# Kernel tuning notes

Measured on AMD Instinct MI355X. Metric: run time of the kernel, lower is better.

Reference implementation:

```python
import jax, jax.numpy as jnp
import numpy as np

B, N, C_IN = 8, 2048, 3
D = 64            # graph-conv feature dim
SPARSE_K = 8      # k_neighbors(16) * sparse_ratio(0.5)
LEVELS = 3        # wavelet_levels
H1, H2 = 256, 128 # fusion hidden dims

def _lin(key, fan_in, fan_out):
    k1, k2 = jax.random.split(key)
    s = 1.0 / np.sqrt(fan_in)
    W = jax.random.uniform(k1, (fan_in, fan_out), minval=-s, maxval=s, dtype=jnp.float32)
    b = jax.random.uniform(k2, (fan_out,), minval=-s, maxval=s, dtype=jnp.float32)
    return W, b

def setup_inputs() -> dict:
    key = jax.random.key(0)
    ks = jax.random.split(key, 12)
    x = jax.random.normal(ks[0], (B, N, C_IN), dtype=jnp.float32)
    W1, b1 = _lin(ks[1], C_IN, D)          # feature_transform
    W2, b2 = _lin(ks[2], 2 * D, D)         # edge_conv
    Ws1, bs1 = _lin(ks[3], C_IN, 64)       # suppressor layer 1
    Ws2, bs2 = _lin(ks[4], 64, LEVELS)     # suppressor layer 2
    Wf1, bf1 = _lin(ks[5], D * LEVELS, H1) # fusion
    Wf2, bf2 = _lin(ks[6], H1, H2)
    Wf3, bf3 = _lin(ks[7], H2, C_IN)
    ones = jnp.ones; zeros = jnp.zeros
    return {
        'x': x,
        'W1': W1, 'b1': b1, 'g1': ones((D,), jnp.float32), 'be1': zeros((D,), jnp.float32),
        'W2': W2, 'b2': b2, 'g2': ones((D,), jnp.float32), 'be2': zeros((D,), jnp.float32),
        'Ws1': Ws1, 'bs1': bs1, 'Ws2': Ws2, 'bs2': bs2,
        'Wf1': Wf1, 'bf1': bf1, 'gf1': ones((H1,), jnp.float32), 'bef1': zeros((H1,), jnp.float32),
        'Wf2': Wf2, 'bf2': bf2, 'gf2': ones((H2,), jnp.float32), 'bef2': zeros((H2,), jnp.float32),
        'Wf3': Wf3, 'bf3': bf3,
    }

def _leaky(v):
    return jnp.where(v > 0, v, 0.2 * v)

def reference(x, W1, b1, g1, be1, W2, b2, g2, be2, Ws1, bs1, Ws2, bs2,
              Wf1, bf1, gf1, bef1, Wf2, bf2, gf2, bef2, Wf3, bf3):
    # ---- AdaptiveSparseGraphConv ----
    # feature transform + eval-mode BN (running mean 0 / var 1 -> affine)
    feat = _leaky((x @ W1 + b1) * g1 + be1)                     # [B,N,D]
    # KNN via squared distances (monotonic in true cdist)
    x2 = jnp.sum(x * x, axis=-1)                                # [B,N]
    d2 = x2[:, :, None] + x2[:, None, :] - 2.0 * jnp.einsum('bnc,bmc->bnm', x, x)
    _, idx = jax.lax.top_k(-d2, SPARSE_K)                       # [B,N,k] nearest
    neighbor = jax.vmap(lambda f, i: f[i])(feat, idx)           # [B,N,k,D]
    edge = jnp.concatenate(
        [jnp.broadcast_to(feat[:, :, None, :], neighbor.shape), neighbor], axis=-1)  # [B,N,k,2D]
    conv = _leaky((edge @ W2 + b2) * g2 + be2)                  # [B,N,k,D]
    agg = jnp.max(conv, axis=2)                                 # [B,N,D]
    # ---- AdaptiveFrequencySupressor (per-point wavelet-level weights) ----
    fw = jax.nn.sigmoid(jax.nn.relu(x @ Ws1 + bs1) @ Ws2 + bs2) # [B,N,LEVELS]
    # frequency-adaptive multi-level weighting, concat across levels
    multi = (agg[:, :, None, :] * fw[:, :, :, None]).reshape(B, N, LEVELS * D)  # [B,N,LEVELS*D]
    # ---- EnhancedMultiScaleFusion (eval: dropout off, BN affine) ----
    h = _leaky((multi @ Wf1 + bf1) * gf1 + bef1)
    h = _leaky((h @ Wf2 + bf2) * gf2 + bef2)
    delta = h @ Wf3 + bf3                                       # [B,N,3]
    # ---- residual regularized output ----
    return x + 0.1 * delta
```

## Files before the change

### kernel.cpp

```cpp
#include <hip/hip_runtime.h>
#include <hip/hip_bf16.h>
#include <math.h>

#define BB   8
#define NN   2048
#define BN   16384
#define KNB  8

__device__ __forceinline__ float leaky(float v){ return v > 0.f ? v : 0.2f*v; }

__device__ __forceinline__ ushort f2bf(float f){
    unsigned u = __float_as_uint(f);
    return (ushort)((u + 0x7FFFu + ((u >> 16) & 1u)) >> 16);
}
__device__ __forceinline__ float bf2f(ushort h){
    return __uint_as_float(((unsigned)h) << 16);
}

using bf16x8 = __attribute__((ext_vector_type(8))) short;
using f32x16 = __attribute__((ext_vector_type(16))) float;

__global__ __launch_bounds__(256) void k_pq(
    const float* __restrict__ x,
    const float* __restrict__ W1, const float* __restrict__ b1,
    const float* __restrict__ g1, const float* __restrict__ be1,
    const float* __restrict__ W2,
    const float* __restrict__ Wf1, const float* __restrict__ Wf2,
    float* __restrict__ P, ushort* __restrict__ Qb,
    ushort* __restrict__ Wf1T, ushort* __restrict__ Wf2T)
{
    int t = threadIdx.x;
    int bid = blockIdx.x;
    if (bid >= 256) {
        if (bid < 280) {
            int base = (bid - 256) * 2048 + t * 8;
            #pragma unroll
            for (int j = 0; j < 8; ++j) {
                int e = base + j;
                int n = e / 192, k = e % 192;
                Wf1T[e] = f2bf(Wf1[k*256 + n]);
            }
        } else {
            int base = (bid - 280) * 2048 + t * 8;
            #pragma unroll
            for (int j = 0; j < 8; ++j) {
                int e = base + j;
                int n = e / 256, k = e % 256;
                Wf2T[e] = f2bf(Wf2[k*128 + n]);
            }
        }
        return;
    }

    __shared__ float F_s[64*66];
    __shared__ float W_s[32*132];

    int rb = bid * 64;

    {
        int d = t & 63, g = t >> 6;
        float w0 = W1[d], w1 = W1[64+d], w2 = W1[128+d];
        float bb = b1[d], gg = g1[d], ee = be1[d];
        #pragma unroll 4
        for (int i = 0; i < 16; ++i) {
            int r = g*16 + i;
            const float* xp = &x[(rb + r)*3];
            float f = xp[0]*w0 + xp[1]*w1 + xp[2]*w2 + bb;
            f = leaky(f*gg + ee);
            F_s[r*66 + d] = f;
        }
    }

    int tx = t & 15, ty = t >> 4;
    float acc[4][8];
    #pragma unroll
    for (int i = 0; i < 4; ++i)
        #pragma unroll
        for (int j = 0; j < 8; ++j) acc[i][j] = 0.f;

    for (int k0 = 0; k0 < 64; k0 += 32) {
        __syncthreads();
        #pragma unroll
        for (int it = 0; it < 2; ++it) {
            int i2 = t + it*256;
            int k = i2 >> 4, c8 = (i2 & 15) * 8;
            const float* src = &W2[(k0 + k + (c8 >= 64 ? 64 : 0))*64 + (c8 & 63)];
            *(float4*)&W_s[k*132 + c8]     = *(const float4*)src;
            *(float4*)&W_s[k*132 + c8 + 4] = *(const float4*)(src + 4);
        }
        __syncthreads();
        #pragma unroll 4
        for (int kk = 0; kk < 32; ++kk) {
            float a[4];
            #pragma unroll
            for (int i = 0; i < 4; ++i) a[i] = F_s[(ty*4 + i)*66 + k0 + kk];
            float4 wA = *(const float4*)&W_s[kk*132 + tx*8];
            float4 wB = *(const float4*)&W_s[kk*132 + tx*8 + 4];
            #pragma unroll
            for (int i = 0; i < 4; ++i) {
                acc[i][0] = fmaf(a[i], wA.x, acc[i][0]);
                acc[i][1] = fmaf(a[i], wA.y, acc[i][1]);
                acc[i][2] = fmaf(a[i], wA.z, acc[i][2]);
                acc[i][3] = fmaf(a[i], wA.w, acc[i][3]);
                acc[i][4] = fmaf(a[i], wB.x, acc[i][4]);
                acc[i][5] = fmaf(a[i], wB.y, acc[i][5]);
                acc[i][6] = fmaf(a[i], wB.z, acc[i][6]);
                acc[i][7] = fmaf(a[i], wB.w, acc[i][7]);
            }
        }
    }

    #pragma unroll
    for (int i = 0; i < 4; ++i) {
        int r = rb + ty*4 + i;
        if (tx < 8) {
            *(float4*)&P[r*64 + tx*8]     = make_float4(acc[i][0], acc[i][1], acc[i][2], acc[i][3]);
            *(float4*)&P[r*64 + tx*8 + 4] = make_float4(acc[i][4], acc[i][5], acc[i][6], acc[i][7]);
        } else {
            union { ushort u[8]; uint4 v; } pk;
            #pragma unroll
            for (int j = 0; j < 8; ++j) pk.u[j] = f2bf(acc[i][j]);
            *(uint4*)&Qb[r*64 + (tx - 8)*8] = pk.v;
        }
    }
}

#define CE64(a, b) { bool c_ = (b) < (a); unsigned long long mn_ = c_ ? (b) : (a); \
                     unsigned long long mx_ = c_ ? (a) : (b); (a) = mn_; (b) = mx_; }

__global__ __launch_bounds__(1024, 8) void k_knn(const float* __restrict__ x, int* __restrict__ idxo)
{
    __shared__ __align__(16) char smem[65536];
    float4*   sp  = (float4*)smem;
    unsigned* khi = (unsigned*)smem;
    unsigned* klo = (unsigned*)(smem + 32768);

    int t = threadIdx.x;
    int b = blockIdx.x >> 6;
    int qbase = (blockIdx.x & 63) * 32;
    int q = t & 31, seg = t >> 5;

    for (int i = t; i < NN; i += 1024) {
        float a = x[(b*NN + i)*3 + 0];
        float c = x[(b*NN + i)*3 + 1];
        float e = x[(b*NN + i)*3 + 2];
        sp[i] = make_float4(a, c, e, a*a + c*c + e*e);
    }
    __syncthreads();

    float4 qv = sp[qbase + q];

    unsigned long long R[8];
    #pragma unroll
    for (int j = 0; j < 8; ++j) R[j] = 0xFFFFFFFFFFFFFFFFull;

    int m0 = seg * 64;
    #pragma unroll 2
    for (int g = 0; g < 8; ++g) {
        unsigned long long S[8];
        #pragma unroll
        for (int jj = 0; jj < 8; ++jj) {
            int m = m0 + g*8 + jj;
            float4 v = sp[m];
            float s = qv.x*v.x; s = fmaf(qv.y, v.y, s); s = fmaf(qv.z, v.z, s);
            float d2 = fmaf(-2.f, s, qv.w + v.w);
            unsigned u = __float_as_uint(fmaxf(d2, 0.f));
            S[jj] = ((unsigned long long)u << 32) | (unsigned)m;
        }
        CE64(S[0],S[1]); CE64(S[2],S[3]); CE64(S[4],S[5]); CE64(S[6],S[7]);
        CE64(S[0],S[2]); CE64(S[1],S[3]); CE64(S[4],S[6]); CE64(S[5],S[7]);
        CE64(S[1],S[2]); CE64(S[5],S[6]);
        CE64(S[0],S[4]); CE64(S[1],S[5]); CE64(S[2],S[6]); CE64(S[3],S[7]);
        CE64(S[2],S[4]); CE64(S[3],S[5]);
        CE64(S[1],S[2]); CE64(S[3],S[4]); CE64(S[5],S[6]);
        #pragma unroll
        for (int j = 0; j < 8; ++j) {
            unsigned long long bb = S[7-j];
            R[j] = R[j] < bb ? R[j] : bb;
        }
        CE64(R[0],R[4]); CE64(R[1],R[5]); CE64(R[2],R[6]); CE64(R[3],R[7]);
        CE64(R[0],R[2]); CE64(R[1],R[3]); CE64(R[4],R[6]); CE64(R[5],R[7]);
        CE64(R[0],R[1]); CE64(R[2],R[3]); CE64(R[4],R[5]); CE64(R[6],R[7]);
    }

    __syncthreads();
    #pragma unroll
    for (int j = 0; j < 8; ++j) {
        khi[j*1024 + t] = (unsigned)(R[j] >> 32);
        klo[j*1024 + t] = (unsigned)R[j];
    }

    for (int L = 32; L >= 2; L >>= 1) {
        __syncthreads();
        unsigned long long A[8], Bv[8];
        int p = t >> 5;
        bool active = (p < (L >> 1));
        if (active) {
            int rowA = (2*p)*32 + q, rowB = (2*p + 1)*32 + q;
            #pragma unroll
            for (int j = 0; j < 8; ++j) {
                A[j]  = ((unsigned long long)khi[j*1024 + rowA] << 32) | klo[j*1024 + rowA];
                Bv[j] = ((unsigned long long)khi[j*1024 + rowB] << 32) | klo[j*1024 + rowB];
            }
        }
        __syncthreads();
        if (active) {
            unsigned long long C[8];
            #pragma unroll
            for (int j = 0; j < 8; ++j) {
                unsigned long long bb = Bv[7-j];
                C[j] = A[j] < bb ? A[j] : bb;
            }
            CE64(C[0],C[4]); CE64(C[1],C[5]); CE64(C[2],C[6]); CE64(C[3],C[7]);
            CE64(C[0],C[2]); CE64(C[1],C[3]); CE64(C[4],C[6]); CE64(C[5],C[7]);
            CE64(C[0],C[1]); CE64(C[2],C[3]); CE64(C[4],C[5]); CE64(C[6],C[7]);
            if (L > 2) {
                int rowO = p*32 + q;
                #pragma unroll
                for (int j = 0; j < 8; ++j) {
                    khi[j*1024 + rowO] = (unsigned)(C[j] >> 32);
                    klo[j*1024 + rowO] = (unsigned)C[j];
                }
            } else {
                #pragma unroll
                for (int j = 0; j < 8; ++j)
                    idxo[(b*NN + qbase + q)*KNB + j] = b*NN + (int)(C[j] & 0xFFFFFFFFu);
            }
        }
    }
}

__global__ __launch_bounds__(256) void k_agg(
    const float* __restrict__ x,
    const float* __restrict__ P, const ushort* __restrict__ Qb,
    const int* __restrict__ idx,
    const float* __restrict__ Ws1, const float* __restrict__ bs1,
    const float* __restrict__ Ws2, const float* __restrict__ bs2,
    const float* __restrict__ b2, const float* __restrict__ g2,
    const float* __restrict__ be2,
    ushort* __restrict__ multi)
{
    int lane = threadIdx.x & 63;
    int p = blockIdx.x * 4 + (threadIdx.x >> 6);

    float x0 = x[p*3+0], x1 = x[p*3+1], x2 = x[p*3+2];
    float h = fmaxf(x0*Ws1[lane] + x1*Ws1[64+lane] + x2*Ws1[128+lane] + bs1[lane], 0.f);
    float s[3];
    #pragma unroll
    for (int l = 0; l < 3; ++l) {
        float v = h * Ws2[lane*3 + l];
        #pragma unroll
        for (int off = 32; off; off >>= 1) v += __shfl_xor(v, off, 64);
        s[l] = v + bs2[l];
    }
    float fw0 = 1.f/(1.f + expf(-s[0]));
    float fw1 = 1.f/(1.f + expf(-s[1]));
    float fw2 = 1.f/(1.f + expf(-s[2]));

    float Pv = P[p*64 + lane] + b2[lane];
    float g = g2[lane], be = be2[lane];
    float mx = -1e30f;
    #pragma unroll
    for (int j = 0; j < KNB; ++j) {
        int nb = idx[p*KNB + j];
        float qv = bf2f(Qb[nb*64 + lane]);
        float v = (Pv + qv) * g + be;
        mx = fmaxf(mx, leaky(v));
    }
    multi[p*192 + lane]       = f2bf(mx * fw0);
    multi[p*192 + 64  + lane] = f2bf(mx * fw1);
    multi[p*192 + 128 + lane] = f2bf(mx * fw2);
}

__global__ __launch_bounds__(256) void k_h1(
    const ushort* __restrict__ multi, const ushort* __restrict__ Wf1T,
    const float* __restrict__ bf1, const float* __restrict__ gf1,
    const float* __restrict__ bef1, ushort* __restrict__ h1)
{
    __shared__ ushort A_s[128*72];
    __shared__ ushort B_s[64*72];

    int t = threadIdx.x, w = t >> 6, lane = t & 63;
    int rb = blockIdx.x * 128, cb = blockIdx.y * 64;

    f32x16 acc[2];
    #pragma unroll
    for (int i = 0; i < 16; ++i) { acc[0][i] = 0.f; acc[1][i] = 0.f; }

    for (int k0 = 0; k0 < 192; k0 += 64) {
        #pragma unroll
        for (int it = 0; it < 4; ++it) {
            int i = t + it*256; int r = i >> 3, kq = (i & 7)*8;
            *(uint4*)&A_s[r*72 + kq] = *(const uint4*)&multi[(rb + r)*192 + k0 + kq];
        }
        #pragma unroll
        for (int it = 0; it < 2; ++it) {
            int i = t + it*256; int n = i >> 3, kq = (i & 7)*8;
            *(uint4*)&B_s[n*72 + kq] = *(const uint4*)&Wf1T[(cb + n)*192 + k0 + kq];
        }
        __syncthreads();
        int row = w*32 + (lane & 31);
        int kb = (lane >> 5)*8;
        #pragma unroll
        for (int s = 0; s < 4; ++s) {
            bf16x8 a  = *(const bf16x8*)&A_s[row*72 + s*16 + kb];
            bf16x8 b0 = *(const bf16x8*)&B_s[(lane & 31)*72 + s*16 + kb];
            bf16x8 b1 = *(const bf16x8*)&B_s[(32 + (lane & 31))*72 + s*16 + kb];
            acc[0] = __builtin_amdgcn_mfma_f32_32x32x16_bf16(a, b0, acc[0], 0, 0, 0);
            acc[1] = __builtin_amdgcn_mfma_f32_32x32x16_bf16(a, b1, acc[1], 0, 0, 0);
        }
        __syncthreads();
    }

    #pragma unroll
    for (int nb = 0; nb < 2; ++nb) {
        int c = cb + nb*32 + (lane & 31);
        float bv = bf1[c], gv = gf1[c], ev = bef1[c];
        #pragma unroll
        for (int r16 = 0; r16 < 16; ++r16) {
            int rr = (r16 & 3) + 8*(r16 >> 2) + 4*(lane >> 5);
            float v = leaky((acc[nb][r16] + bv)*gv + ev);
            h1[(rb + w*32 + rr)*256 + c] = f2bf(v);
        }
    }
}

__global__ __launch_bounds__(256) void k_h2out(
    const ushort* __restrict__ h1, const ushort* __restrict__ Wf2T,
    const float* __restrict__ bf2, const float* __restrict__ gf2,
    const float* __restrict__ bef2,
    const float* __restrict__ Wf3, const float* __restrict__ bf3,
    const float* __restrict__ x, float* __restrict__ out)
{
    __shared__ ushort A_s[128*72];
    __shared__ ushort B_s[128*72];

    int t = threadIdx.x, w = t >> 6, lane = t & 63;
    int rb = blockIdx.x * 128;

    f32x16 acc[4];
    #pragma unroll
    for (int nb = 0; nb < 4; ++nb)
        #pragma unroll
        for (int i = 0; i < 16; ++i) acc[nb][i] = 0.f;

    for (int k0 = 0; k0 < 256; k0 += 64) {
        #pragma unroll
        for (int it = 0; it < 4; ++it) {
            int i = t + it*256; int r = i >> 3, kq = (i & 7)*8;
            *(uint4*)&A_s[r*72 + kq] = *(const uint4*)&h1[(rb + r)*256 + k0 + kq];
        }
        #pragma unroll
        for (int it = 0; it < 4; ++it) {
            int i = t + it*256; int n = i >> 3, kq = (i & 7)*8;
            *(uint4*)&B_s[n*72 + kq] = *(const uint4*)&Wf2T[n*256 + k0 + kq];
        }
        __syncthreads();
        int row = w*32 + (lane & 31);
        int kb = (lane >> 5)*8;
        #pragma unroll
        for (int s = 0; s < 4; ++s) {
            bf16x8 a = *(const bf16x8*)&A_s[row*72 + s*16 + kb];
            #pragma unroll
            for (int nb = 0; nb < 4; ++nb) {
                bf16x8 b = *(const bf16x8*)&B_s[(nb*32 + (lane & 31))*72 + s*16 + kb];
                acc[nb] = __builtin_amdgcn_mfma_f32_32x32x16_bf16(a, b, acc[nb], 0, 0, 0);
            }
        }
        __syncthreads();
    }

    float bv[4], gv[4], ev[4], w3[4][3];
    #pragma unroll
    for (int nb = 0; nb < 4; ++nb) {
        int c = nb*32 + (lane & 31);
        bv[nb] = bf2[c]; gv[nb] = gf2[c]; ev[nb] = bef2[c];
        #pragma unroll
        for (int l = 0; l < 3; ++l) w3[nb][l] = Wf3[c*3 + l];
    }
    float b30 = bf3[0], b31 = bf3[1], b32 = bf3[2];

    #pragma unroll
    for (int r16 = 0; r16 < 16; ++r16) {
        float d0 = 0.f, d1 = 0.f, d2 = 0.f;
        #pragma unroll
        for (int nb = 0; nb < 4; ++nb) {
            float v = leaky((acc[nb][r16] + bv[nb])*gv[nb] + ev[nb]);
            d0 = fmaf(v, w3[nb][0], d0);
            d1 = fmaf(v, w3[nb][1], d1);
            d2 = fmaf(v, w3[nb][2], d2);
        }
        #pragma unroll
        for (int off = 16; off; off >>= 1) {
            d0 += __shfl_xor(d0, off, 64);
            d1 += __shfl_xor(d1, off, 64);
            d2 += __shfl_xor(d2, off, 64);
        }
        int row = rb + w*32 + (r16 & 3) + 8*(r16 >> 2) + 4*(lane >> 5);
        int l = lane & 31;
        if (l < 3) {
            float dl = (l == 0) ? d0 : (l == 1 ? d1 : d2);
            float bl = (l == 0) ? b30 : (l == 1 ? b31 : b32);
            out[row*3 + l] = x[row*3 + l] + 0.1f*(dl + bl);
        }
    }
}

extern "C" void kernel_launch(void* const* d_in, const int* in_sizes, int n_in,
                              void* d_out, int out_size, void* d_ws, size_t ws_size,
                              hipStream_t stream)
{
    const float* x    = (const float*)d_in[0];
    const float* W1   = (const float*)d_in[1];
    const float* b1   = (const float*)d_in[2];
    const float* g1   = (const float*)d_in[3];
    const float* be1  = (const float*)d_in[4];
    const float* W2   = (const float*)d_in[5];
    const float* b2   = (const float*)d_in[6];
    const float* g2   = (const float*)d_in[7];
    const float* be2  = (const float*)d_in[8];
    const float* Ws1  = (const float*)d_in[9];
    const float* bs1  = (const float*)d_in[10];
    const float* Ws2  = (const float*)d_in[11];
    const float* bs2  = (const float*)d_in[12];
    const float* Wf1  = (const float*)d_in[13];
    const float* bf1  = (const float*)d_in[14];
    const float* gf1  = (const float*)d_in[15];
    const float* bef1 = (const float*)d_in[16];
    const float* Wf2  = (const float*)d_in[17];
    const float* bf2  = (const float*)d_in[18];
    const float* gf2  = (const float*)d_in[19];
    const float* bef2 = (const float*)d_in[20];
    const float* Wf3  = (const float*)d_in[21];
    const float* bf3  = (const float*)d_in[22];
    float* out = (float*)d_out;

    char* ws = (char*)d_ws;
    int*    idx   = (int*)   (ws + 0);
    ushort* Wf1T  = (ushort*)(ws + (1u << 20));
    ushort* Wf2T  = (ushort*)(ws + (1u << 20) + (512u << 10));
    float*  P     = (float*) (ws + (2u  << 20));
    ushort* Qb    = (ushort*)(ws + (6u  << 20));
    ushort* multi = (ushort*)(ws + (8u  << 20));
    ushort* h1    = (ushort*)(ws + (14u << 20));

    k_pq<<<296, 256, 0, stream>>>(x, W1, b1, g1, be1, W2, Wf1, Wf2, P, Qb, Wf1T, Wf2T);
    k_knn<<<BB*64, 1024, 0, stream>>>(x, idx);
    k_agg<<<BN/4, 256, 0, stream>>>(x, P, Qb, idx, Ws1, bs1, Ws2, bs2, b2, g2, be2, multi);
    k_h1<<<dim3(BN/128, 4), 256, 0, stream>>>(multi, Wf1T, bf1, gf1, bef1, h1);
    k_h2out<<<dim3(BN/128, 1), 256, 0, stream>>>(h1, Wf2T, bf2, gf2, bef2, Wf3, bf3, x, out);
}
```

Before: 176.7 us.

## Fuse aggregation, fusion MLP layers and output into one kernel

Merges the neighbor-max aggregation, the first fusion GEMM, the second GEMM and the output projection into a single kernel that handles 64 rows per block and keeps the multi-level features and h1 in shared memory. This removes the global writes and reads of the intermediate multi and h1 tensors and two kernel launches. In exchange each block uses about 60KB of LDS, which limits occupancy. Every block also reloads the full Wf1T and Wf2T weights, and the aggregation phase now runs serially over 16 rows per wave.

New measurement: 172.1 us. 2.6% less time.

```diff
diff --git a/kernel.cpp b/kernel.cpp
--- a/kernel.cpp
+++ b/kernel.cpp
@@ -230,7 +230,7 @@
     }
 }
 
-__global__ __launch_bounds__(256) void k_agg(
+__global__ __launch_bounds__(256) void k_fuse(
     const float* __restrict__ x,
     const float* __restrict__ P, const ushort* __restrict__ Qb,
     const int* __restrict__ idx,
@@ -238,157 +238,146 @@
     const float* __restrict__ Ws2, const float* __restrict__ bs2,
     const float* __restrict__ b2, const float* __restrict__ g2,
     const float* __restrict__ be2,
-    ushort* __restrict__ multi)
+    const ushort* __restrict__ Wf1T, const float* __restrict__ bf1,
+    const float* __restrict__ gf1, const float* __restrict__ bef1,
+    const ushort* __restrict__ Wf2T, const float* __restrict__ bf2,
+    const float* __restrict__ gf2, const float* __restrict__ bef2,
+    const float* __restrict__ Wf3, const float* __restrict__ bf3,
+    float* __restrict__ out)
 {
-    int lane = threadIdx.x & 63;
-    int p = blockIdx.x * 4 + (threadIdx.x >> 6);
-
-    float x0 = x[p*3+0], x1 = x[p*3+1], x2 = x[p*3+2];
-    float h = fmaxf(x0*Ws1[lane] + x1*Ws1[64+lane] + x2*Ws1[128+lane] + bs1[lane], 0.f);
-    float s[3];
-    #pragma unroll
-    for (int l = 0; l < 3; ++l) {
-        float v = h * Ws2[lane*3 + l];
-        #pragma unroll
-        for (int off = 32; off; off >>= 1) v += __shfl_xor(v, off, 64);
-        s[l] = v + bs2[l];
-    }
-    float fw0 = 1.f/(1.f + expf(-s[0]));
-    float fw1 = 1.f/(1.f + expf(-s[1]));
-    float fw2 = 1.f/(1.f + expf(-s[2]));
-
-    float Pv = P[p*64 + lane] + b2[lane];
-    float g = g2[lane], be = be2[lane];
-    float mx = -1e30f;
-    #pragma unroll
-    for (int j = 0; j < KNB; ++j) {
-        int nb = idx[p*KNB + j];
-        float qv = bf2f(Qb[nb*64 + lane]);
-        float v = (Pv + qv) * g + be;
-        mx = fmaxf(mx, leaky(v));
-    }
-    multi[p*192 + lane]       = f2bf(mx * fw0);
-    multi[p*192 + 64  + lane] = f2bf(mx * fw1);
-    multi[p*192 + 128 + lane] = f2bf(mx * fw2);
-}
-
-__global__ __launch_bounds__(256) void k_h1(
-    const ushort* __restrict__ multi, const ushort* __restrict__ Wf1T,
-    const float* __restrict__ bf1, const float* __restrict__ gf1,
-    const float* __restrict__ bef1, ushort* __restrict__ h1)
-{
-    __shared__ ushort A_s[128*72];
-    __shared__ ushort B_s[64*72];
+    __shared__ __align__(16) char smem[60928];
+    ushort* A_s  = (ushort*)smem;
+    ushort* B_s  = (ushort*)(smem + 25600);
+    ushort* h1_s = (ushort*)smem;
+    ushort* B2_s = (ushort*)(smem + 40960);
+    float*  pd   = (float*) (smem + 59392);
 
     int t = threadIdx.x, w = t >> 6, lane = t & 63;
-    int rb = blockIdx.x * 128, cb = blockIdx.y * 64;
-
-    f32x16 acc[2];
-    #pragma unroll
-    for (int i = 0; i < 16; ++i) { acc[0][i] = 0.f; acc[1][i] = 0.f; }
+    int rb = blockIdx.x * 64;
+
+    {
+        float ws1a = Ws1[lane], ws1b = Ws1[64+lane], ws1c = Ws1[128+lane];
+        float bs1v = bs1[lane];
+        float ws2a = Ws2[lane*3+0], ws2b = Ws2[lane*3+1], ws2c = Ws2[lane*3+2];
+        float bs20 = bs2[0], bs21 = bs2[1], bs22 = bs2[2];
+        float g2v = g2[lane], be2v = be2[lane], b2v = b2[lane];
+        for (int i = 0; i < 16; ++i) {
+            int r = w*16 + i, p = rb + r;
+            float x0 = x[p*3+0], x1 = x[p*3+1], x2 = x[p*3+2];
+            float h = fmaxf(fmaf(x2, ws1c, fmaf(x1, ws1b, fmaf(x0, ws1a, bs1v))), 0.f);
+            float s0 = h*ws2a, s1 = h*ws2b, s2 = h*ws2c;
+            #pragma unroll
+            for (int off = 32; off; off >>= 1) {
+                s0 += __shfl_xor(s0, off, 64);
+                s1 += __shfl_xor(s1, off, 64);
+                s2 += __shfl_xor(s2, off, 64);
+            }
+            float fw0 = 1.f/(1.f + expf(-(s0 + bs20)));
+            float fw1 = 1.f/(1.f + expf(-(s1 + bs21)));
+            float fw2 = 1.f/(1.f + expf(-(s2 + bs22)));
+            float Pv = P[p*64 + lane] + b2v;
+            float mx = -1e30f;
+            #pragma unroll
+            for (int j = 0; j < KNB; ++j) {
+                int nb = idx[p*KNB + j];
+                float qv = bf2f(Qb[nb*64 + lane]);
+                mx = fmaxf(mx, leaky((Pv + qv)*g2v + be2v));
+            }
+            A_s[r*200 + lane]       = f2bf(mx * fw0);
+            A_s[r*200 + 64 + lane]  = f2bf(mx * fw1);
+            A_s[r*200 + 128 + lane] = f2bf(mx * fw2);
+        }
+    }
+
+    int rg = w >> 1;
+    int nh = (w & 1) * 128;
+    int l31 = lane & 31, kb = (lane >> 5) * 8;
+    int row = rg*32 + l31;
+
+    f32x16 acc[4];
+    #pragma unroll
+    for (int n2 = 0; n2 < 4; ++n2)
+        #pragma unroll
+        for (int i = 0; i < 16; ++i) acc[n2][i] = 0.f;
 
     for (int k0 = 0; k0 < 192; k0 += 64) {
-        #pragma unroll
-        for (int it = 0; it < 4; ++it) {
-            int i = t + it*256; int r = i >> 3, kq = (i & 7)*8;
-            *(uint4*)&A_s[r*72 + kq] = *(const uint4*)&multi[(rb + r)*192 + k0 + kq];
-        }
-        #pragma unroll
-        for (int it = 0; it < 2; ++it) {
-            int i = t + it*256; int n = i >> 3, kq = (i & 7)*8;
-            *(uint4*)&B_s[n*72 + kq] = *(const uint4*)&Wf1T[(cb + n)*192 + k0 + kq];
-        }
-        __syncthreads();
-        int row = w*32 + (lane & 31);
-        int kb = (lane >> 5)*8;
+        __syncthreads();
+        #pragma unroll
+        for (int it = 0; it < 8; ++it) {
+            int i = t + it*256;
+            int n = i >> 3, kq = (i & 7)*8;
+            *(uint4*)&B_s[n*72 + kq] = *(const uint4*)&Wf1T[n*192 + k0 + kq];
+        }
+        __syncthreads();
         #pragma unroll
         for (int s = 0; s < 4; ++s) {
-            bf16x8 a  = *(const bf16x8*)&A_s[row*72 + s*16 + kb];
-            bf16x8 b0 = *(const bf16x8*)&B_s[(lane & 31)*72 + s*16 + kb];
-            bf16x8 b1 = *(const bf16x8*)&B_s[(32 + (lane & 31))*72 + s*16 + kb];
-            acc[0] = __builtin_amdgcn_mfma_f32_32x32x16_bf16(a, b0, acc[0], 0, 0, 0);
-            acc[1] = __builtin_amdgcn_mfma_f32_32x32x16_bf16(a, b1, acc[1], 0, 0, 0);
-        }
-        __syncthreads();
-    }
-
-    #pragma unroll
-    for (int nb = 0; nb < 2; ++nb) {
-        int c = cb + nb*32 + (lane & 31);
+            bf16x8 a = *(const bf16x8*)&A_s[row*200 + k0 + s*16 + kb];
+            #pragma unroll
+            for (int n2 = 0; n2 < 4; ++n2) {
+                bf16x8 b = *(const bf16x8*)&B_s[(nh + n2*32 + l31)*72 + s*16 + kb];
+                acc[n2] = __builtin_amdgcn_mfma_f32_32x32x16_bf16(a, b, acc[n2], 0, 0, 0);
+            }
+        }
+    }
+    __syncthreads();
+
+    #pragma unroll
+    for (int n2 = 0; n2 < 4; ++n2) {
+        int c = nh + n2*32 + l31;
         float bv = bf1[c], gv = gf1[c], ev = bef1[c];
         #pragma unroll
         for (int r16 = 0; r16 < 16; ++r16) {
             int rr = (r16 & 3) + 8*(r16 >> 2) + 4*(lane >> 5);
-            float v = leaky((acc[nb][r16] + bv)*gv + ev);
-            h1[(rb + w*32 + rr)*256 + c] = f2bf(v);
-        }
-    }
-}
-
-__global__ __launch_bounds__(256) void k_h2out(
-    const ushort* __restrict__ h1, const ushort* __restrict__ Wf2T,
-    const float* __restrict__ bf2, const float* __restrict__ gf2,
-    const float* __restrict__ bef2,
-    const float* __restrict__ Wf3, const float* __restrict__ bf3,
-    const float* __restrict__ x, float* __restrict__ out)
-{
-    __shared__ ushort A_s[128*72];
-    __shared__ ushort B_s[128*72];
-
-    int t = threadIdx.x, w = t >> 6, lane = t & 63;
-    int rb = blockIdx.x * 128;
-
-    f32x16 acc[4];
-    #pragma unroll
-    for (int nb = 0; nb < 4; ++nb)
-        #pragma unroll
-        for (int i = 0; i < 16; ++i) acc[nb][i] = 0.f;
+            float v = leaky((acc[n2][r16] + bv)*gv + ev);
+            h1_s[(rg*32 + rr)*264 + c] = f2bf(v);
+        }
+    }
+
+    int ch = (w & 1) * 64;
+    f32x16 acc2[2];
+    #pragma unroll
+    for (int n2 = 0; n2 < 2; ++n2)
+        #pragma unroll
+        for (int i = 0; i < 16; ++i) acc2[n2][i] = 0.f;
 
     for (int k0 = 0; k0 < 256; k0 += 64) {
+        __syncthreads();
         #pragma unroll
         for (int it = 0; it < 4; ++it) {
-            int i = t + it*256; int r = i >> 3, kq = (i & 7)*8;
-            *(uint4*)&A_s[r*72 + kq] = *(const uint4*)&h1[(rb + r)*256 + k0 + kq];
-        }
-        #pragma unroll
-        for (int it = 0; it < 4; ++it) {
-            int i = t + it*256; int n = i >> 3, kq = (i & 7)*8;
-            *(uint4*)&B_s[n*72 + kq] = *(const uint4*)&Wf2T[n*256 + k0 + kq];
-        }
-        __syncthreads();
-        int row = w*32 + (lane & 31);
-        int kb = (lane >> 5)*8;
+            int i = t + it*256;
+            int n = i >> 3, kq = (i & 7)*8;
+            *(uint4*)&B2_s[n*72 + kq] = *(const uint4*)&Wf2T[n*256 + k0 + kq];
+        }
+        __syncthreads();
         #pragma unroll
         for (int s = 0; s < 4; ++s) {
-            bf16x8 a = *(const bf16x8*)&A_s[row*72 + s*16 + kb];
-            #pragma unroll
-            for (int nb = 0; nb < 4; ++nb) {
-                bf16x8 b = *(const bf16x8*)&B_s[(nb*32 + (lane & 31))*72 + s*16 + kb];
-                acc[nb] = __builtin_amdgcn_mfma_f32_32x32x16_bf16(a, b, acc[nb], 0, 0, 0);
-            }
-        }
-        __syncthreads();
-    }
-
-    float bv[4], gv[4], ev[4], w3[4][3];
-    #pragma unroll
-    for (int nb = 0; nb < 4; ++nb) {
-        int c = nb*32 + (lane & 31);
-        bv[nb] = bf2[c]; gv[nb] = gf2[c]; ev[nb] = bef2[c];
-        #pragma unroll
-        for (int l = 0; l < 3; ++l) w3[nb][l] = Wf3[c*3 + l];
-    }
-    float b30 = bf3[0], b31 = bf3[1], b32 = bf3[2];
-
+            bf16x8 a = *(const bf16x8*)&h1_s[row*264 + k0 + s*16 + kb];
+            #pragma unroll
+            for (int n2 = 0; n2 < 2; ++n2) {
+                bf16x8 b = *(const bf16x8*)&B2_s[(ch + n2*32 + l31)*72 + s*16 + kb];
+                acc2[n2] = __builtin_amdgcn_mfma_f32_32x32x16_bf16(a, b, acc2[n2], 0, 0, 0);
+            }
+        }
+    }
+
+    float bv[2], gv[2], ev[2], w3[2][3];
+    #pragma unroll
+    for (int n2 = 0; n2 < 2; ++n2) {
+        int c = ch + n2*32 + l31;
+        bv[n2] = bf2[c]; gv[n2] = gf2[c]; ev[n2] = bef2[c];
+        #pragma unroll
+        for (int l = 0; l < 3; ++l) w3[n2][l] = Wf3[c*3 + l];
+    }
+    __syncthreads();
     #pragma unroll
     for (int r16 = 0; r16 < 16; ++r16) {
         float d0 = 0.f, d1 = 0.f, d2 = 0.f;
         #pragma unroll
-        for (int nb = 0; nb < 4; ++nb) {
-            float v = leaky((acc[nb][r16] + bv[nb])*gv[nb] + ev[nb]);
-            d0 = fmaf(v, w3[nb][0], d0);
-            d1 = fmaf(v, w3[nb][1], d1);
-            d2 = fmaf(v, w3[nb][2], d2);
+        for (int n2 = 0; n2 < 2; ++n2) {
+            float v = leaky((acc2[n2][r16] + bv[n2])*gv[n2] + ev[n2]);
+            d0 = fmaf(v, w3[n2][0], d0);
+            d1 = fmaf(v, w3[n2][1], d1);
+            d2 = fmaf(v, w3[n2][2], d2);
         }
         #pragma unroll
         for (int off = 16; off; off >>= 1) {
@@ -396,13 +385,18 @@
             d1 += __shfl_xor(d1, off, 64);
             d2 += __shfl_xor(d2, off, 64);
         }
-        int row = rb + w*32 + (r16 & 3) + 8*(r16 >> 2) + 4*(lane >> 5);
-        int l = lane & 31;
-        if (l < 3) {
-            float dl = (l == 0) ? d0 : (l == 1 ? d1 : d2);
-            float bl = (l == 0) ? b30 : (l == 1 ? b31 : b32);
-            out[row*3 + l] = x[row*3 + l] + 0.1f*(dl + bl);
-        }
+        int rr = rg*32 + (r16 & 3) + 8*(r16 >> 2) + 4*(lane >> 5);
+        if (l31 < 3) {
+            float dl = (l31 == 0) ? d0 : (l31 == 1 ? d1 : d2);
+            pd[(rr*2 + (w & 1))*3 + l31] = dl;
+        }
+    }
+    __syncthreads();
+
+    if (t < 192) {
+        int r = t / 3, l = t - r*3;
+        float delta = pd[(r*2 + 0)*3 + l] + pd[(r*2 + 1)*3 + l] + bf3[l];
+        out[(rb + r)*3 + l] = x[(rb + r)*3 + l] + 0.1f*delta;
     }
 }
 
@@ -441,12 +435,10 @@
     ushort* Wf2T  = (ushort*)(ws + (1u << 20) + (512u << 10));
     float*  P     = (float*) (ws + (2u  << 20));
     ushort* Qb    = (ushort*)(ws + (6u  << 20));
-    ushort* multi = (ushort*)(ws + (8u  << 20));
-    ushort* h1    = (ushort*)(ws + (14u << 20));
 
     k_pq<<<296, 256, 0, stream>>>(x, W1, b1, g1, be1, W2, Wf1, Wf2, P, Qb, Wf1T, Wf2T);
     k_knn<<<BB*64, 1024, 0, stream>>>(x, idx);
-    k_agg<<<BN/4, 256, 0, stream>>>(x, P, Qb, idx, Ws1, bs1, Ws2, bs2, b2, g2, be2, multi);
-    k_h1<<<dim3(BN/128, 4), 256, 0, stream>>>(multi, Wf1T, bf1, gf1, bef1, h1);
-    k_h2out<<<dim3(BN/128, 1), 256, 0, stream>>>(h1, Wf2T, bf2, gf2, bef2, Wf3, bf3, x, out);
-}
+    k_fuse<<<BN/64, 256, 0, stream>>>(x, P, Qb, idx, Ws1, bs1, Ws2, bs2, b2, g2, be2,
+                                      Wf1T, bf1, gf1, bef1, Wf2T, bf2, gf2, bef2,
+                                      Wf3, bf3, out);
+}
```
